# Optimization experiments

Measured on AMD Instinct MI355X. Metric: run time of the kernel, lower is better.

## Reference

```python
import jax, jax.numpy as jnp
import numpy as np

T, B, D = 256, 256, 512
H, DK = 8, 64          # num_heads, d_kv; inner_dim = H*DK = 512
NUM_GROUPS = 16


def setup_inputs() -> dict:
    key = jax.random.key(0)
    ks = jax.random.split(key, 6)
    hidden_states = jax.random.normal(ks[0], (T, B, D), dtype=jnp.float32)
    # sorted group ids over the batch axis (what _infer_group_ids_from_mask recovers)
    group_ids = jnp.sort(jax.random.randint(ks[1], (B,), 0, NUM_GROUPS, dtype=jnp.int32))
    scale = 1.0 / np.sqrt(D)
    Wq = jax.random.normal(ks[2], (D, H * DK), dtype=jnp.float32) * scale
    Wk = jax.random.normal(ks[3], (D, H * DK), dtype=jnp.float32) * scale
    Wv = jax.random.normal(ks[4], (D, H * DK), dtype=jnp.float32) * scale
    Wo = jax.random.normal(ks[5], (H * DK, D), dtype=jnp.float32) * scale
    return {"hidden_states": hidden_states, "group_ids": group_ids,
            "Wq": Wq, "Wk": Wk, "Wv": Wv, "Wo": Wo}


def reference(hidden_states, group_ids, Wq, Wk, Wv, Wo):
    # Group-restricted self-attention along the batch axis, per time step & head.
    # Equivalent to the block-sparse MiniFlash kernel: entries attend only to
    # batch entries with the same group id.
    t, b, d = hidden_states.shape
    q = (hidden_states @ Wq).reshape(t, b, H, DK)
    k = (hidden_states @ Wk).reshape(t, b, H, DK)
    v = (hidden_states @ Wv).reshape(t, b, H, DK)
    sm_scale = 1.0 / np.sqrt(DK)
    # scores: [T, H, B, B] over the batch axis
    scores = jnp.einsum("tihd,tjhd->thij", q, k) * sm_scale
    allowed = group_ids[:, None] == group_ids[None, :]          # [B, B]
    neg = jnp.finfo(scores.dtype).min
    scores = jnp.where(allowed[None, None, :, :], scores, neg)
    attn = jax.nn.softmax(scores, axis=-1)
    out = jnp.einsum("thij,tjhd->tihd", attn, v).reshape(t, b, H * DK)
    return out @ Wo
```

## Files before the change

kernel.cpp:

```cpp
#include <hip/hip_runtime.h>
#include <hip/hip_bf16.h>

typedef __attribute__((ext_vector_type(8))) short short8;
typedef __attribute__((ext_vector_type(4))) short short4v;
typedef __attribute__((ext_vector_type(4))) float f32x4;

#define MFMA16(a, b, c) __builtin_amdgcn_mfma_f32_16x16x32_bf16(a, b, c, 0, 0, 0)

__device__ __forceinline__ unsigned short f2bf(float f) {
    union { __hip_bfloat16 h; unsigned short u; } v;
    v.h = __float2bfloat16(f);
    return v.u;
}

__device__ __forceinline__ short8 pack8(float4 a, float4 b) {
    short8 p;
    p[0] = (short)f2bf(a.x); p[1] = (short)f2bf(a.y);
    p[2] = (short)f2bf(a.z); p[3] = (short)f2bf(a.w);
    p[4] = (short)f2bf(b.x); p[5] = (short)f2bf(b.y);
    p[6] = (short)f2bf(b.z); p[7] = (short)f2bf(b.w);
    return p;
}

__device__ __forceinline__ int swz64(int row, int bytecol) {
    return row * 64 + ((bytecol ^ ((row & 7) << 4)) >> 1);
}
__device__ __forceinline__ int swz256(int row, int bytecol) {
    return row * 256 + ((bytecol ^ ((row & 7) << 4)) >> 1);
}

__global__ __launch_bounds__(256) void wprep(
    const float* __restrict__ Wq, const float* __restrict__ Wk,
    const float* __restrict__ Wv, const float* __restrict__ Wo,
    unsigned short* __restrict__ wt)
{
    __shared__ float tile[64][65];
    const int bid = blockIdx.x;
    const int m = bid >> 6, tb = bid & 63;
    const int kr = (tb >> 3) << 6, nc = (tb & 7) << 6;
    const float* W = (m == 0) ? Wq : (m == 1) ? Wk : (m == 2) ? Wv : Wo;
    const int tid = threadIdx.x;
    for (int i = tid; i < 4096; i += 256)
        tile[i >> 6][i & 63] = W[(size_t)(kr + (i >> 6)) * 512 + nc + (i & 63)];
    __syncthreads();
    unsigned short* dst = wt + (size_t)m * 262144;
    for (int i = tid; i < 4096; i += 256)
        dst[(size_t)(nc + (i >> 6)) * 512 + kr + (i & 63)] = f2bf(tile[i & 63][i >> 6]);
}

__global__ __launch_bounds__(1024, 4) void qkv_gemm(
    const float* __restrict__ hs,
    const unsigned short* __restrict__ wt,
    unsigned short* __restrict__ qkvb)
{
    __shared__ unsigned short As[128 * 40];
    __shared__ unsigned short Bts[512 * 40];

    const int orig = blockIdx.x;
    const int wg = (orig & 7) * 192 + (orig >> 3);
    const int mb = wg / 3;
    const int nb = wg - mb * 3;

    const int tid  = threadIdx.x;
    const int lane = tid & 63;
    const int w    = tid >> 6;
    const int l15  = lane & 15;
    const int hi4  = lane >> 4;
    const int wr   = w >> 2, wc = w & 3;

    f32x4 acc[2][8];
    #pragma unroll
    for (int m = 0; m < 2; ++m)
        #pragma unroll
        for (int n = 0; n < 8; ++n)
            acc[m][n] = (f32x4){0.f, 0.f, 0.f, 0.f};

    const bool isA = tid < 512;
    const int bn = tid & 511;
    const int ai = bn >> 2, aq = bn & 3;

    const float* __restrict__ asrc = hs + ((size_t)mb * 128 + ai) * 512 + aq * 8;
    const unsigned short* __restrict__ bsrc = wt + ((size_t)nb * 512 + bn) * 512;

    float4 af0, af1;
    short8 b8[4];
    if (isA) {
        af0 = *(const float4*)asrc; af1 = *(const float4*)(asrc + 4);
    } else {
        #pragma unroll
        for (int q = 0; q < 4; ++q) b8[q] = *(const short8*)(bsrc + q * 8);
    }

    for (int kb = 0; kb < 512; kb += 32) {
        if (isA) *(short8*)&As[ai * 40 + aq * 8] = pack8(af0, af1);
        else {
            #pragma unroll
            for (int q = 0; q < 4; ++q) *(short8*)&Bts[bn * 40 + q * 8] = b8[q];
        }
        __syncthreads();
        if (kb < 480) {
            const int kn = kb + 32;
            if (isA) {
                af0 = *(const float4*)(asrc + kn);
                af1 = *(const float4*)(asrc + kn + 4);
            } else {
                #pragma unroll
                for (int q = 0; q < 4; ++q)
                    b8[q] = *(const short8*)(bsrc + kn + q * 8);
            }
        }
        short8 afr[2];
        #pragma unroll
        for (int m = 0; m < 2; ++m)
            afr[m] = *(const short8*)&As[(wr * 32 + m * 16 + l15) * 40 + hi4 * 8];
        __builtin_amdgcn_s_setprio(1);
        #pragma unroll
        for (int n = 0; n < 8; ++n) {
            const short8 bfr = *(const short8*)&Bts[(wc * 128 + n * 16 + l15) * 40 + hi4 * 8];
            #pragma unroll
            for (int m = 0; m < 2; ++m)
                acc[m][n] = MFMA16(afr[m], bfr, acc[m][n]);
        }
        __builtin_amdgcn_s_setprio(0);
        __syncthreads();
    }

    const size_t matoff = (size_t)nb * 33554432;
    #pragma unroll
    for (int m = 0; m < 2; ++m) {
        #pragma unroll
        for (int n = 0; n < 8; ++n) {
            const int col = wc * 128 + n * 16 + l15;
            const int hh = col >> 6, d = col & 63;
            #pragma unroll
            for (int r = 0; r < 4; ++r) {
                const int row = mb * 128 + wr * 32 + m * 16 + hi4 * 4 + r;
                const int t = row >> 8, i = row & 255;
                qkvb[matoff + (((size_t)t * 8 + hh) << 14) + (i << 6) + d] =
                    f2bf(acc[m][n][r]);
            }
        }
    }
}

__global__ __launch_bounds__(1024, 4) void attn_split(
    const unsigned short* __restrict__ qkvb,
    const int* __restrict__ gid,
    float* __restrict__ out)
{
    __shared__ unsigned short Ksh[256 * 64];
    __shared__ unsigned short Vt[64 * 256];
    __shared__ unsigned short Ps[256 * 64];
    __shared__ int sgid[256];
    __shared__ int glo[16], ghi[16];

    const int th = blockIdx.x;
    const int t = th >> 3, h = th & 7;
    const int tid  = threadIdx.x;
    const int lane = tid & 63;
    const int w    = tid >> 6;
    const int l15  = lane & 15;
    const int hi4  = lane >> 4;
    const int wrow = w << 4;

    if (tid < 16) { glo[tid] = 256; ghi[tid] = -1; }
    __syncthreads();
    if (tid < 256) {
        const int g = gid[tid];
        sgid[tid] = g;
        atomicMin(&glo[g], tid);
        atomicMax(&ghi[g], tid);
    }

    const unsigned short* __restrict__ qb = qkvb + ((size_t)th << 14);
    const unsigned short* __restrict__ kb = qkvb + 33554432ull + ((size_t)th << 14);
    const unsigned short* __restrict__ vb = qkvb + 67108864ull + ((size_t)th << 14);

    {
        const int kr = tid >> 2, kq = tid & 3;
        const short8 k0 = *(const short8*)(kb + kr * 64 + kq * 16);
        const short8 k1 = *(const short8*)(kb + kr * 64 + kq * 16 + 8);
        *(short8*)&Ksh[swz64(kr, kq * 32)]      = k0;
        *(short8*)&Ksh[swz64(kr, kq * 32 + 16)] = k1;
        const short8 v0 = *(const short8*)(vb + kr * 64 + kq * 16);
        const short8 v1 = *(const short8*)(vb + kr * 64 + kq * 16 + 8);
        *(short8*)&Ps[kr * 64 + kq * 16]     = v0;
        *(short8*)&Ps[kr * 64 + kq * 16 + 8] = v1;
    }
    short8 qf[2];
    #pragma unroll
    for (int ks = 0; ks < 2; ++ks)
        qf[ks] = *(const short8*)(qb + (wrow + l15) * 64 + ks * 32 + hi4 * 8);
    __syncthreads();

    {
        const int d = tid & 63, jc = tid >> 6;
        short8 a, b;
        #pragma unroll
        for (int jj = 0; jj < 8; ++jj) a[jj] = Ps[(jc * 16 + jj) * 64 + d];
        #pragma unroll
        for (int jj = 0; jj < 8; ++jj) b[jj] = Ps[(jc * 16 + 8 + jj) * 64 + d];
        *(short8*)&Vt[swz256(d, jc * 32)]      = a;
        *(short8*)&Vt[swz256(d, jc * 32 + 16)] = b;
    }
    __syncthreads();

    int rg[4];
    #pragma unroll
    for (int r = 0; r < 4; ++r) rg[r] = sgid[wrow + hi4 * 4 + r];
    const int klo = glo[sgid[wrow]];
    const int khi = ghi[sgid[wrow + 15]];

    f32x4 o[4];
    float mrun[4], lrun[4];
    #pragma unroll
    for (int n = 0; n < 4; ++n) o[n] = (f32x4){0.f, 0.f, 0.f, 0.f};
    #pragma unroll
    for (int r = 0; r < 4; ++r) { mrun[r] = -3.0e38f; lrun[r] = 0.f; }

    for (int kc = klo & ~63; kc <= khi; kc += 64) {
        f32x4 sfr[4];
        __builtin_amdgcn_s_setprio(1);
        #pragma unroll
        for (int n = 0; n < 4; ++n) {
            const int krow = kc + n * 16 + l15;
            const short8 kf0 = *(const short8*)&Ksh[swz64(krow, hi4 * 16)];
            const short8 kf1 = *(const short8*)&Ksh[swz64(krow, 64 + hi4 * 16)];
            f32x4 z = (f32x4){0.f, 0.f, 0.f, 0.f};
            z = MFMA16(qf[0], kf0, z);
            z = MFMA16(qf[1], kf1, z);
            sfr[n] = z;
        }
        __builtin_amdgcn_s_setprio(0);
        int cg[4];
        #pragma unroll
        for (int n = 0; n < 4; ++n) cg[n] = sgid[kc + n * 16 + l15];

        #pragma unroll
        for (int r = 0; r < 4; ++r) {
            const int gr = rg[r];
            float sv[4];
            float smax = -3.0e38f;
            #pragma unroll
            for (int n = 0; n < 4; ++n) {
                float x = sfr[n][r] * 0.125f;
                x = (cg[n] == gr) ? x : -3.0e38f;
                sv[n] = x;
                smax = fmaxf(smax, x);
            }
            smax = fmaxf(smax, __shfl_xor(smax, 1));
            smax = fmaxf(smax, __shfl_xor(smax, 2));
            smax = fmaxf(smax, __shfl_xor(smax, 4));
            smax = fmaxf(smax, __shfl_xor(smax, 8));
            const float newm = fmaxf(mrun[r], smax);
            const float corr = __expf(mrun[r] - newm);
            float ps = 0.f;
            unsigned short pb[4];
            #pragma unroll
            for (int n = 0; n < 4; ++n) {
                const float p = (sv[n] > -1.0e38f) ? __expf(sv[n] - newm) : 0.f;
                ps += p;
                pb[n] = f2bf(p);
            }
            ps += __shfl_xor(ps, 1); ps += __shfl_xor(ps, 2);
            ps += __shfl_xor(ps, 4); ps += __shfl_xor(ps, 8);
            lrun[r] = lrun[r] * corr + ps;
            mrun[r] = newm;
            #pragma unroll
            for (int n = 0; n < 4; ++n) o[n][r] *= corr;
            const int prow = wrow + hi4 * 4 + r;
            #pragma unroll
            for (int n = 0; n < 4; ++n)
                Ps[swz64(prow, (n * 16 + l15) * 2)] = pb[n];
        }

        const short8 pa0 = *(const short8*)&Ps[swz64(wrow + l15, hi4 * 16)];
        const short8 pa1 = *(const short8*)&Ps[swz64(wrow + l15, 64 + hi4 * 16)];
        __builtin_amdgcn_s_setprio(1);
        #pragma unroll
        for (int n = 0; n < 4; ++n) {
            const short8 vb0 = *(const short8*)&Vt[swz256(n * 16 + l15, (kc + hi4 * 8) * 2)];
            const short8 vb1 = *(const short8*)&Vt[swz256(n * 16 + l15, (kc + 32 + hi4 * 8) * 2)];
            o[n] = MFMA16(pa0, vb0, o[n]);
            o[n] = MFMA16(pa1, vb1, o[n]);
        }
        __builtin_amdgcn_s_setprio(0);
    }

    float* __restrict__ op = out + (size_t)t * (256 * 512) + h * 64;
    #pragma unroll
    for (int r = 0; r < 4; ++r) {
        const int row = wrow + hi4 * 4 + r;
        const float inv = 1.0f / lrun[r];
        #pragma unroll
        for (int n = 0; n < 4; ++n)
            op[(size_t)row * 512 + n * 16 + l15] = o[n][r] * inv;
    }
}

__global__ __launch_bounds__(1024, 4) void qkv_attn_mfma(
    const float* __restrict__ hs,
    const int*   __restrict__ gid,
    const float* __restrict__ Wq, const float* __restrict__ Wk,
    const float* __restrict__ Wv,
    const unsigned short* __restrict__ wt,
    float*       __restrict__ out)
{
    __shared__ unsigned short Xs[256 * 64];
    __shared__ unsigned short Wsh[192 * 64];
    __shared__ unsigned short Ksh[256 * 64];
    __shared__ unsigned short Vt[64 * 256];
    __shared__ unsigned short XP[256 * 64];
    __shared__ int sgid[256];
    __shared__ int glo[16], ghi[16];

    const int bid = blockIdx.x;
    const int h   = (bid & 63) >> 3;
    const int t   = ((bid >> 6) << 3) + (bid & 7);

    const int tid  = threadIdx.x;
    const int lane = tid & 63;
    const int w    = tid >> 6;
    const int l15  = lane & 15;
    const int hi4  = lane >> 4;
    const int mg   = w & 3;
    const int ng   = w >> 2;

    if (tid < 16) { glo[tid] = 256; ghi[tid] = -1; }
    __syncthreads();
    if (tid < 256) {
        const int g = gid[tid];
        sgid[tid] = g;
        atomicMin(&glo[g], tid);
        atomicMax(&ghi[g], tid);
    }

    const float* __restrict__ Xbase = hs + (size_t)t * (256 * 512);

    const int xr = tid >> 2, xq = tid & 3;
    const bool doW = tid < 768;
    const int wc = tid >> 2;
    const int wq = tid & 3;
    const int wmat = wc >> 6, wcol = wc & 63;
    const unsigned short* __restrict__ wsrc =
        wt ? wt + ((size_t)wmat * 512 + h * 64 + wcol) * 512 : nullptr;
    const float* __restrict__ wfsrc =
        (wmat == 0) ? Wq : (wmat == 1) ? Wk : Wv;

    f32x4 acc[4][3];
    #pragma unroll
    for (int mt = 0; mt < 4; ++mt)
        #pragma unroll
        for (int nt = 0; nt < 3; ++nt)
            acc[mt][nt] = (f32x4){0.f, 0.f, 0.f, 0.f};

    float4 xf[4];
    short8 w8[2];
    {
        const float* s = Xbase + (size_t)xr * 512 + xq * 16;
        xf[0] = *(const float4*)(s + 0);  xf[1] = *(const float4*)(s + 4);
        xf[2] = *(const float4*)(s + 8);  xf[3] = *(const float4*)(s + 12);
        if (doW) {
            if (wt) {
                w8[0] = *(const short8*)(wsrc + wq * 16);
                w8[1] = *(const short8*)(wsrc + wq * 16 + 8);
            } else {
                #pragma unroll
                for (int b = 0; b < 2; ++b)
                    #pragma unroll
                    for (int j = 0; j < 8; ++j)
                        w8[b][j] = (short)f2bf(
                            wfsrc[(size_t)(wq * 16 + b * 8 + j) * 512 + h * 64 + wcol]);
            }
        }
    }

    for (int kb = 0; kb < 512; kb += 64) {
        *(short8*)&Xs[swz64(xr, xq * 32 + 0)]  = pack8(xf[0], xf[1]);
        *(short8*)&Xs[swz64(xr, xq * 32 + 16)] = pack8(xf[2], xf[3]);
        if (doW) {
            *(short8*)&Wsh[swz64(wc, wq * 32 + 0)]  = w8[0];
            *(short8*)&Wsh[swz64(wc, wq * 32 + 16)] = w8[1];
        }
        __syncthreads();
        if (kb < 448) {
            const int kn = kb + 64;
            const float* s = Xbase + (size_t)xr * 512 + kn + xq * 16;
            xf[0] = *(const float4*)(s + 0);  xf[1] = *(const float4*)(s + 4);
            xf[2] = *(const float4*)(s + 8);  xf[3] = *(const float4*)(s + 12);
            if (doW) {
                if (wt) {
                    w8[0] = *(const short8*)(wsrc + kn + wq * 16);
                    w8[1] = *(const short8*)(wsrc + kn + wq * 16 + 8);
                } else {
                    #pragma unroll
                    for (int b = 0; b < 2; ++b)
                        #pragma unroll
                        for (int j = 0; j < 8; ++j)
                            w8[b][j] = (short)f2bf(
                                wfsrc[(size_t)(kn + wq * 16 + b * 8 + j) * 512 + h * 64 + wcol]);
                }
            }
        }
        #pragma unroll
        for (int ks = 0; ks < 2; ++ks) {
            short8 af[4];
            #pragma unroll
            for (int mt = 0; mt < 4; ++mt)
                af[mt] = *(const short8*)&Xs[swz64(mg * 64 + mt * 16 + l15,
                                                   ks * 64 + hi4 * 16)];
            __builtin_amdgcn_s_setprio(1);
            #pragma unroll
            for (int nt = 0; nt < 3; ++nt) {
                const short8 bf = *(const short8*)&Wsh[swz64(ng * 48 + nt * 16 + l15,
                                                             ks * 64 + hi4 * 16)];
                #pragma unroll
                for (int mt = 0; mt < 4; ++mt)
                    acc[mt][nt] = MFMA16(af[mt], bf, acc[mt][nt]);
            }
            __builtin_amdgcn_s_setprio(0);
        }
        __syncthreads();
    }

    #pragma unroll
    for (int nt = 0; nt < 3; ++nt) {
        const int c0 = (ng * 3 + nt) * 16;
        const int m  = c0 >> 6;
        const int d0 = c0 & 63;
        #pragma unroll
        for (int mt = 0; mt < 4; ++mt) {
            const int rowb = mg * 64 + mt * 16 + hi4 * 4;
            if (m == 0) {
                #pragma unroll
                for (int r = 0; r < 4; ++r)
                    XP[swz64(rowb + r, (d0 + l15) * 2)] = f2bf(acc[mt][nt][r]);
            } else if (m == 1) {
                #pragma unroll
                for (int r = 0; r < 4; ++r)
                    Ksh[swz64(rowb + r, (d0 + l15) * 2)] = f2bf(acc[mt][nt][r]);
            } else {
                short4v vv;
                #pragma unroll
                for (int r = 0; r < 4; ++r) vv[r] = (short)f2bf(acc[mt][nt][r]);
                *(short4v*)&Vt[swz256(d0 + l15, rowb * 2)] = vv;
            }
        }
    }
    __syncthreads();

    const int wrow = w << 4;
    int rg[4];
    #pragma unroll
    for (int r = 0; r < 4; ++r) rg[r] = sgid[wrow + hi4 * 4 + r];
    const int klo = glo[sgid[wrow]];
    const int khi = ghi[sgid[wrow + 15]];

    short8 qf[2];
    #pragma unroll
    for (int ks = 0; ks < 2; ++ks)
        qf[ks] = *(const short8*)&XP[swz64(wrow + l15, ks * 64 + hi4 * 16)];

    f32x4 o[4];
    float mrun[4], lrun[4];
    #pragma unroll
    for (int n = 0; n < 4; ++n) o[n] = (f32x4){0.f, 0.f, 0.f, 0.f};
    #pragma unroll
    for (int r = 0; r < 4; ++r) { mrun[r] = -3.0e38f; lrun[r] = 0.f; }

    for (int kc = klo & ~63; kc <= khi; kc += 64) {
        f32x4 sfr[4];
        __builtin_amdgcn_s_setprio(1);
        #pragma unroll
        for (int n = 0; n < 4; ++n) {
            const int krow = kc + n * 16 + l15;
            const short8 kf0 = *(const short8*)&Ksh[swz64(krow, hi4 * 16)];
            const short8 kf1 = *(const short8*)&Ksh[swz64(krow, 64 + hi4 * 16)];
            f32x4 z = (f32x4){0.f, 0.f, 0.f, 0.f};
            z = MFMA16(qf[0], kf0, z);
            z = MFMA16(qf[1], kf1, z);
            sfr[n] = z;
        }
        __builtin_amdgcn_s_setprio(0);
        int cg[4];
        #pragma unroll
        for (int n = 0; n < 4; ++n) cg[n] = sgid[kc + n * 16 + l15];

        #pragma unroll
        for (int r = 0; r < 4; ++r) {
            const int gr = rg[r];
            float sv[4];
            float smax = -3.0e38f;
            #pragma unroll
            for (int n = 0; n < 4; ++n) {
                float x = sfr[n][r] * 0.125f;
                x = (cg[n] == gr) ? x : -3.0e38f;
                sv[n] = x;
                smax = fmaxf(smax, x);
            }
            smax = fmaxf(smax, __shfl_xor(smax, 1));
            smax = fmaxf(smax, __shfl_xor(smax, 2));
            smax = fmaxf(smax, __shfl_xor(smax, 4));
            smax = fmaxf(smax, __shfl_xor(smax, 8));
            const float newm = fmaxf(mrun[r], smax);
            const float corr = __expf(mrun[r] - newm);
            float ps = 0.f;
            unsigned short pb[4];
            #pragma unroll
            for (int n = 0; n < 4; ++n) {
                const float p = (sv[n] > -1.0e38f) ? __expf(sv[n] - newm) : 0.f;
                ps += p;
                pb[n] = f2bf(p);
            }
            ps += __shfl_xor(ps, 1); ps += __shfl_xor(ps, 2);
            ps += __shfl_xor(ps, 4); ps += __shfl_xor(ps, 8);
            lrun[r] = lrun[r] * corr + ps;
            mrun[r] = newm;
            #pragma unroll
            for (int n = 0; n < 4; ++n) o[n][r] *= corr;
            const int prow = wrow + hi4 * 4 + r;
            #pragma unroll
            for (int n = 0; n < 4; ++n)
                XP[swz64(prow, (n * 16 + l15) * 2)] = pb[n];
        }

        const short8 pa0 = *(const short8*)&XP[swz64(wrow + l15, hi4 * 16)];
        const short8 pa1 = *(const short8*)&XP[swz64(wrow + l15, 64 + hi4 * 16)];
        __builtin_amdgcn_s_setprio(1);
        #pragma unroll
        for (int n = 0; n < 4; ++n) {
            const short8 vb0 = *(const short8*)&Vt[swz256(n * 16 + l15, (kc + hi4 * 8) * 2)];
            const short8 vb1 = *(const short8*)&Vt[swz256(n * 16 + l15, (kc + 32 + hi4 * 8) * 2)];
            o[n] = MFMA16(pa0, vb0, o[n]);
            o[n] = MFMA16(pa1, vb1, o[n]);
        }
        __builtin_amdgcn_s_setprio(0);
    }

    float* __restrict__ op = out + (size_t)t * (256 * 512) + h * 64;
    #pragma unroll
    for (int r = 0; r < 4; ++r) {
        const int row = wrow + hi4 * 4 + r;
        const float inv = 1.0f / lrun[r];
        #pragma unroll
        for (int n = 0; n < 4; ++n)
            op[(size_t)row * 512 + n * 16 + l15] = o[n][r] * inv;
    }
}

__global__ __launch_bounds__(1024, 4) void oproj_mfma(
    const float* __restrict__ Wo,
    const unsigned short* __restrict__ wot,
    float* __restrict__ out)
{
    __shared__ unsigned short As[128 * 40];
    __shared__ unsigned short Bts[512 * 40];

    const int tid  = threadIdx.x;
    const int lane = tid & 63;
    const int w    = tid >> 6;
    const int l15  = lane & 15;
    const int hi4  = lane >> 4;
    const int wr   = w >> 2;
    const int wc   = w & 3;
    const size_t r0 = (size_t)blockIdx.x * 128;

    f32x4 acc[2][8];
    #pragma unroll
    for (int m = 0; m < 2; ++m)
        #pragma unroll
        for (int n = 0; n < 8; ++n)
            acc[m][n] = (f32x4){0.f, 0.f, 0.f, 0.f};

    const bool isA = tid < 512;
    const int bn = tid & 511;
    const int ai = bn >> 2, aq = bn & 3;

    float4 af0, af1;
    short8 b8[4];

    if (isA) {
        const float* s = out + (r0 + ai) * 512 + aq * 8;
        af0 = *(const float4*)s; af1 = *(const float4*)(s + 4);
    } else {
        if (wot) {
            #pragma unroll
            for (int q = 0; q < 4; ++q)
                b8[q] = *(const short8*)(wot + (size_t)bn * 512 + q * 8);
        } else {
            #pragma unroll
            for (int q = 0; q < 4; ++q)
                #pragma unroll
                for (int j = 0; j < 8; ++j)
                    b8[q][j] = (short)f2bf(Wo[(size_t)(q * 8 + j) * 512 + bn]);
        }
    }

    for (int kb = 0; kb < 512; kb += 32) {
        if (isA) *(short8*)&As[ai * 40 + aq * 8] = pack8(af0, af1);
        else {
            #pragma unroll
            for (int q = 0; q < 4; ++q)
                *(short8*)&Bts[bn * 40 + q * 8] = b8[q];
        }
        __syncthreads();
        if (kb < 480) {
            const int kn = kb + 32;
            if (isA) {
                const float* s = out + (r0 + ai) * 512 + kn + aq * 8;
                af0 = *(const float4*)s; af1 = *(const float4*)(s + 4);
            } else {
                if (wot) {
                    #pragma unroll
                    for (int q = 0; q < 4; ++q)
                        b8[q] = *(const short8*)(wot + (size_t)bn * 512 + kn + q * 8);
                } else {
                    #pragma unroll
                    for (int q = 0; q < 4; ++q)
                        #pragma unroll
                        for (int j = 0; j < 8; ++j)
                            b8[q][j] = (short)f2bf(Wo[(size_t)(kn + q * 8 + j) * 512 + bn]);
                }
            }
        }
        short8 afr[2];
        #pragma unroll
        for (int m = 0; m < 2; ++m)
            afr[m] = *(const short8*)&As[(wr * 32 + m * 16 + l15) * 40 + hi4 * 8];
        __builtin_amdgcn_s_setprio(1);
        #pragma unroll
        for (int n = 0; n < 8; ++n) {
            const short8 bfr = *(const short8*)&Bts[(wc * 128 + n * 16 + l15) * 40 + hi4 * 8];
            #pragma unroll
            for (int m = 0; m < 2; ++m)
                acc[m][n] = MFMA16(afr[m], bfr, acc[m][n]);
        }
        __builtin_amdgcn_s_setprio(0);
        __syncthreads();
    }

    #pragma unroll
    for (int m = 0; m < 2; ++m)
        #pragma unroll
        for (int n = 0; n < 8; ++n)
            #pragma unroll
            for (int r = 0; r < 4; ++r)
                out[(r0 + wr * 32 + m * 16 + hi4 * 4 + r) * 512 + wc * 128 + n * 16 + l15] =
                    acc[m][n][r];
}

extern "C" void kernel_launch(void* const* d_in, const int* in_sizes, int n_in,
                              void* d_out, int out_size, void* d_ws, size_t ws_size,
                              hipStream_t stream) {
    const float* hs  = (const float*)d_in[0];
    const int*   gid = (const int*)  d_in[1];
    const float* Wq  = (const float*)d_in[2];
    const float* Wk  = (const float*)d_in[3];
    const float* Wv  = (const float*)d_in[4];
    const float* Wo  = (const float*)d_in[5];
    float* outp = (float*)d_out;

    const size_t WT_SHORTS  = 1048576;
    const size_t QKV_SHORTS = 100663296;
    unsigned short* wt   = nullptr;
    unsigned short* wot  = nullptr;
    unsigned short* qkvb = nullptr;
    if (ws_size >= WT_SHORTS * 2) {
        wt  = (unsigned short*)d_ws;
        wot = wt + (size_t)3 * 262144;
        wprep<<<256, 256, 0, stream>>>(Wq, Wk, Wv, Wo, wt);
        if (ws_size >= (WT_SHORTS + QKV_SHORTS) * 2)
            qkvb = wt + WT_SHORTS;
    }

    if (qkvb) {
        qkv_gemm<<<1536, 1024, 0, stream>>>(hs, wt, qkvb);
        attn_split<<<2048, 1024, 0, stream>>>(qkvb, gid, outp);
    } else {
        qkv_attn_mfma<<<2048, 1024, 0, stream>>>(hs, gid, Wq, Wk, Wv, wt, outp);
    }
    oproj_mfma<<<512, 1024, 0, stream>>>(Wo, wot, outp);
}
```

Before: 370.7 us.

## Retile QKV GEMM, store row-major QKV, pass bf16 attention output to O-proj

The QKV GEMM now uses a K-step of 64 with swizzled LDS tiles and a 2x8 warp layout with 4x4 MFMA tiles per warp. It writes Q/K/V in plain row-major [row, 512] order, and the attention kernel reads that layout with a 512 stride. When the workspace is large enough, attention writes its output as bf16 into a separate buffer, and the output projection reads that buffer directly instead of reloading fp32 and converting. The aim is fewer barriers and better LDS reuse in the GEMM, plus half the intermediate traffic between attention and O-proj. The cost is a larger workspace requirement and a strided, less contiguous Q/K/V read in attention.

```diff
diff --git a/kernel.cpp b/kernel.cpp
--- a/kernel.cpp
+++ b/kernel.cpp
@@ -48,13 +48,13 @@
         dst[(size_t)(nc + (i >> 6)) * 512 + kr + (i & 63)] = f2bf(tile[i & 63][i >> 6]);
 }
 
-__global__ __launch_bounds__(1024, 4) void qkv_gemm(
+__global__ __launch_bounds__(1024, 4) void qkv_gemm2(
     const float* __restrict__ hs,
     const unsigned short* __restrict__ wt,
     unsigned short* __restrict__ qkvb)
 {
-    __shared__ unsigned short As[128 * 40];
-    __shared__ unsigned short Bts[512 * 40];
+    __shared__ unsigned short As[128 * 64];
+    __shared__ unsigned short Bts[512 * 64];
 
     const int orig = blockIdx.x;
     const int wg = (orig & 7) * 192 + (orig >> 3);
@@ -66,78 +66,74 @@
     const int w    = tid >> 6;
     const int l15  = lane & 15;
     const int hi4  = lane >> 4;
-    const int wr   = w >> 2, wc = w & 3;
-
-    f32x4 acc[2][8];
-    #pragma unroll
-    for (int m = 0; m < 2; ++m)
-        #pragma unroll
-        for (int n = 0; n < 8; ++n)
-            acc[m][n] = (f32x4){0.f, 0.f, 0.f, 0.f};
-
-    const bool isA = tid < 512;
-    const int bn = tid & 511;
-    const int ai = bn >> 2, aq = bn & 3;
-
-    const float* __restrict__ asrc = hs + ((size_t)mb * 128 + ai) * 512 + aq * 8;
-    const unsigned short* __restrict__ bsrc = wt + ((size_t)nb * 512 + bn) * 512;
-
-    float4 af0, af1;
+    const int wr   = w >> 3;
+    const int wc   = w & 7;
+
+    f32x4 acc[4][4];
+    #pragma unroll
+    for (int mt = 0; mt < 4; ++mt)
+        #pragma unroll
+        for (int nt = 0; nt < 4; ++nt)
+            acc[mt][nt] = (f32x4){0.f, 0.f, 0.f, 0.f};
+
+    const int ar = tid >> 3, aq = tid & 7;
+    const int bc = tid >> 1, bh = tid & 1;
+    const float* __restrict__ asrc = hs + ((size_t)mb * 128 + ar) * 512 + aq * 8;
+    const unsigned short* __restrict__ bsrc =
+        wt + ((size_t)nb * 512 + bc) * 512 + bh * 32;
+
+    float4 a0, a1;
     short8 b8[4];
-    if (isA) {
-        af0 = *(const float4*)asrc; af1 = *(const float4*)(asrc + 4);
-    } else {
-        #pragma unroll
-        for (int q = 0; q < 4; ++q) b8[q] = *(const short8*)(bsrc + q * 8);
-    }
-
-    for (int kb = 0; kb < 512; kb += 32) {
-        if (isA) *(short8*)&As[ai * 40 + aq * 8] = pack8(af0, af1);
-        else {
-            #pragma unroll
-            for (int q = 0; q < 4; ++q) *(short8*)&Bts[bn * 40 + q * 8] = b8[q];
-        }
+    a0 = *(const float4*)asrc;
+    a1 = *(const float4*)(asrc + 4);
+    #pragma unroll
+    for (int q = 0; q < 4; ++q) b8[q] = *(const short8*)(bsrc + q * 8);
+
+    for (int kb = 0; kb < 512; kb += 64) {
+        *(short8*)&As[swz64(ar, aq * 16)] = pack8(a0, a1);
+        #pragma unroll
+        for (int q = 0; q < 4; ++q)
+            *(short8*)&Bts[swz64(bc, bh * 64 + q * 16)] = b8[q];
         __syncthreads();
-        if (kb < 480) {
-            const int kn = kb + 32;
-            if (isA) {
-                af0 = *(const float4*)(asrc + kn);
-                af1 = *(const float4*)(asrc + kn + 4);
-            } else {
+        if (kb < 448) {
+            const int kn = kb + 64;
+            a0 = *(const float4*)(asrc + kn);
+            a1 = *(const float4*)(asrc + kn + 4);
+            #pragma unroll
+            for (int q = 0; q < 4; ++q)
+                b8[q] = *(const short8*)(bsrc + kn + q * 8);
+        }
+        #pragma unroll
+        for (int ks = 0; ks < 2; ++ks) {
+            short8 af[4];
+            #pragma unroll
+            for (int mt = 0; mt < 4; ++mt)
+                af[mt] = *(const short8*)&As[swz64(wr * 64 + mt * 16 + l15,
+                                                   ks * 64 + hi4 * 16)];
+            __builtin_amdgcn_s_setprio(1);
+            #pragma unroll
+            for (int nt = 0; nt < 4; ++nt) {
+                const short8 bf = *(const short8*)&Bts[swz64(wc * 64 + nt * 16 + l15,
+                                                             ks * 64 + hi4 * 16)];
                 #pragma unroll
-                for (int q = 0; q < 4; ++q)
-                    b8[q] = *(const short8*)(bsrc + kn + q * 8);
-            }
-        }
-        short8 afr[2];
-        #pragma unroll
-        for (int m = 0; m < 2; ++m)
-            afr[m] = *(const short8*)&As[(wr * 32 + m * 16 + l15) * 40 + hi4 * 8];
-        __builtin_amdgcn_s_setprio(1);
-        #pragma unroll
-        for (int n = 0; n < 8; ++n) {
-            const short8 bfr = *(const short8*)&Bts[(wc * 128 + n * 16 + l15) * 40 + hi4 * 8];
-            #pragma unroll
-            for (int m = 0; m < 2; ++m)
-                acc[m][n] = MFMA16(afr[m], bfr, acc[m][n]);
-        }
-        __builtin_amdgcn_s_setprio(0);
+                for (int mt = 0; mt < 4; ++mt)
+                    acc[mt][nt] = MFMA16(af[mt], bf, acc[mt][nt]);
+            }
+            __builtin_amdgcn_s_setprio(0);
+        }
         __syncthreads();
     }
 
-    const size_t matoff = (size_t)nb * 33554432;
-    #pragma unroll
-    for (int m = 0; m < 2; ++m) {
-        #pragma unroll
-        for (int n = 0; n < 8; ++n) {
-            const int col = wc * 128 + n * 16 + l15;
-            const int hh = col >> 6, d = col & 63;
+    unsigned short* __restrict__ dst = qkvb + (size_t)nb * 33554432ull;
+    #pragma unroll
+    for (int mt = 0; mt < 4; ++mt) {
+        #pragma unroll
+        for (int nt = 0; nt < 4; ++nt) {
+            const int col = wc * 64 + nt * 16 + l15;
             #pragma unroll
             for (int r = 0; r < 4; ++r) {
-                const int row = mb * 128 + wr * 32 + m * 16 + hi4 * 4 + r;
-                const int t = row >> 8, i = row & 255;
-                qkvb[matoff + (((size_t)t * 8 + hh) << 14) + (i << 6) + d] =
-                    f2bf(acc[m][n][r]);
+                const int row = mb * 128 + wr * 64 + mt * 16 + hi4 * 4 + r;
+                dst[(size_t)row * 512 + col] = f2bf(acc[mt][nt][r]);
             }
         }
     }
@@ -146,6 +142,7 @@
 __global__ __launch_bounds__(1024, 4) void attn_split(
     const unsigned short* __restrict__ qkvb,
     const int* __restrict__ gid,
+    unsigned short* __restrict__ abuf,
     float* __restrict__ out)
 {
     __shared__ unsigned short Ksh[256 * 64];
@@ -172,25 +169,26 @@
         atomicMax(&ghi[g], tid);
     }
 
-    const unsigned short* __restrict__ qb = qkvb + ((size_t)th << 14);
-    const unsigned short* __restrict__ kb = qkvb + 33554432ull + ((size_t)th << 14);
-    const unsigned short* __restrict__ vb = qkvb + 67108864ull + ((size_t)th << 14);
+    const size_t rowbase = (size_t)t * 256 * 512 + h * 64;
+    const unsigned short* __restrict__ qb = qkvb + rowbase;
+    const unsigned short* __restrict__ kbp = qkvb + 33554432ull + rowbase;
+    const unsigned short* __restrict__ vbp = qkvb + 67108864ull + rowbase;
 
     {
         const int kr = tid >> 2, kq = tid & 3;
-        const short8 k0 = *(const short8*)(kb + kr * 64 + kq * 16);
-        const short8 k1 = *(const short8*)(kb + kr * 64 + kq * 16 + 8);
+        const short8 k0 = *(const short8*)(kbp + (size_t)kr * 512 + kq * 16);
+        const short8 k1 = *(const short8*)(kbp + (size_t)kr * 512 + kq * 16 + 8);
         *(short8*)&Ksh[swz64(kr, kq * 32)]      = k0;
         *(short8*)&Ksh[swz64(kr, kq * 32 + 16)] = k1;
-        const short8 v0 = *(const short8*)(vb + kr * 64 + kq * 16);
-        const short8 v1 = *(const short8*)(vb + kr * 64 + kq * 16 + 8);
+        const short8 v0 = *(const short8*)(vbp + (size_t)kr * 512 + kq * 16);
+        const short8 v1 = *(const short8*)(vbp + (size_t)kr * 512 + kq * 16 + 8);
         *(short8*)&Ps[kr * 64 + kq * 16]     = v0;
         *(short8*)&Ps[kr * 64 + kq * 16 + 8] = v1;
     }
     short8 qf[2];
     #pragma unroll
     for (int ks = 0; ks < 2; ++ks)
-        qf[ks] = *(const short8*)(qb + (wrow + l15) * 64 + ks * 32 + hi4 * 8);
+        qf[ks] = *(const short8*)(qb + (size_t)(wrow + l15) * 512 + ks * 32 + hi4 * 8);
     __syncthreads();
 
     {
@@ -287,14 +285,26 @@
         __builtin_amdgcn_s_setprio(0);
     }
 
-    float* __restrict__ op = out + (size_t)t * (256 * 512) + h * 64;
-    #pragma unroll
-    for (int r = 0; r < 4; ++r) {
-        const int row = wrow + hi4 * 4 + r;
-        const float inv = 1.0f / lrun[r];
-        #pragma unroll
-        for (int n = 0; n < 4; ++n)
-            op[(size_t)row * 512 + n * 16 + l15] = o[n][r] * inv;
+    if (abuf) {
+        unsigned short* __restrict__ op = abuf + rowbase;
+        #pragma unroll
+        for (int r = 0; r < 4; ++r) {
+            const int row = wrow + hi4 * 4 + r;
+            const float inv = 1.0f / lrun[r];
+            #pragma unroll
+            for (int n = 0; n < 4; ++n)
+                op[(size_t)row * 512 + n * 16 + l15] = f2bf(o[n][r] * inv);
+        }
+    } else {
+        float* __restrict__ op = out + rowbase;
+        #pragma unroll
+        for (int r = 0; r < 4; ++r) {
+            const int row = wrow + hi4 * 4 + r;
+            const float inv = 1.0f / lrun[r];
+            #pragma unroll
+            for (int n = 0; n < 4; ++n)
+                op[(size_t)row * 512 + n * 16 + l15] = o[n][r] * inv;
+        }
     }
 }
 
@@ -551,6 +561,7 @@
 __global__ __launch_bounds__(1024, 4) void oproj_mfma(
     const float* __restrict__ Wo,
     const unsigned short* __restrict__ wot,
+    const unsigned short* __restrict__ abuf,
     float* __restrict__ out)
 {
     __shared__ unsigned short As[128 * 40];
@@ -577,11 +588,16 @@
     const int ai = bn >> 2, aq = bn & 3;
 
     float4 af0, af1;
+    short8 a8;
     short8 b8[4];
 
     if (isA) {
-        const float* s = out + (r0 + ai) * 512 + aq * 8;
-        af0 = *(const float4*)s; af1 = *(const float4*)(s + 4);
+        if (abuf) {
+            a8 = *(const short8*)(abuf + (r0 + ai) * 512 + aq * 8);
+        } else {
+            const float* s = out + (r0 + ai) * 512 + aq * 8;
+            af0 = *(const float4*)s; af1 = *(const float4*)(s + 4);
+        }
     } else {
         if (wot) {
             #pragma unroll
@@ -597,7 +613,7 @@
     }
 
     for (int kb = 0; kb < 512; kb += 32) {
-        if (isA) *(short8*)&As[ai * 40 + aq * 8] = pack8(af0, af1);
+        if (isA) *(short8*)&As[ai * 40 + aq * 8] = abuf ? a8 : pack8(af0, af1);
         else {
             #pragma unroll
             for (int q = 0; q < 4; ++q)
@@ -607,8 +623,12 @@
         if (kb < 480) {
             const int kn = kb + 32;
             if (isA) {
-                const float* s = out + (r0 + ai) * 512 + kn + aq * 8;
-                af0 = *(const float4*)s; af1 = *(const float4*)(s + 4);
+                if (abuf) {
+                    a8 = *(const short8*)(abuf + (r0 + ai) * 512 + kn + aq * 8);
+                } else {
+                    const float* s = out + (r0 + ai) * 512 + kn + aq * 8;
+                    af0 = *(const float4*)s; af1 = *(const float4*)(s + 4);
+                }
             } else {
                 if (wot) {
                     #pragma unroll
@@ -660,24 +680,28 @@
     const float* Wo  = (const float*)d_in[5];
     float* outp = (float*)d_out;
 
-    const size_t WT_SHORTS  = 1048576;
-    const size_t QKV_SHORTS = 100663296;
+    const size_t WT_S  = 1048576;
+    const size_t QKV_S = 100663296;
+    const size_t AB_S  = 33554432;
     unsigned short* wt   = nullptr;
     unsigned short* wot  = nullptr;
     unsigned short* qkvb = nullptr;
-    if (ws_size >= WT_SHORTS * 2) {
+    unsigned short* abuf = nullptr;
+    if (ws_size >= WT_S * 2) {
         wt  = (unsigned short*)d_ws;
         wot = wt + (size_t)3 * 262144;
         wprep<<<256, 256, 0, stream>>>(Wq, Wk, Wv, Wo, wt);
-        if (ws_size >= (WT_SHORTS + QKV_SHORTS) * 2)
-            qkvb = wt + WT_SHORTS;
+        if (ws_size >= (WT_S + QKV_S) * 2)
+            qkvb = wt + WT_S;
+        if (ws_size >= (WT_S + QKV_S + AB_S) * 2)
+            abuf = wt + WT_S + QKV_S;
     }
 
     if (qkvb) {
-        qkv_gemm<<<1536, 1024, 0, stream>>>(hs, wt, qkvb);
-        attn_split<<<2048, 1024, 0, stream>>>(qkvb, gid, outp);
+        qkv_gemm2<<<1536, 1024, 0, stream>>>(hs, wt, qkvb);
+        attn_split<<<2048, 1024, 0, stream>>>(qkvb, gid, abuf, outp);
     } else {
         qkv_attn_mfma<<<2048, 1024, 0, stream>>>(hs, gid, Wq, Wk, Wv, wt, outp);
     }
-    oproj_mfma<<<512, 1024, 0, stream>>>(Wo, wot, outp);
-}
+    oproj_mfma<<<512, 1024, 0, stream>>>(Wo, wot, abuf, outp);
+}
```

Measured after the change: 351.8 us. 1.05x faster.
